# Kernel optimization log

Measured on AMD Instinct MI355X. Metric: run time of the kernel, lower is better.

Reference implementation:

```python
import jax, jax.numpy as jnp
import numpy as np

N = 1_000_000  # total_voxels
V = 128        # volume_size


def setup_inputs() -> dict:
    key = jax.random.key(0)
    ks = jax.random.split(key, 10)
    inds = jax.random.randint(ks[0], (N, 3), 0, V, dtype=jnp.int32)
    reference_values = jax.random.normal(ks[1], (1, N), dtype=jnp.float32)
    # SIREN-ish init scales: ~1/sqrt(fan_in) keeps sin() inputs O(1); tiny final
    # layer scale keeps delta_coords sub-voxel (as training would).
    W0 = jax.random.normal(ks[2], (3 * N, 8), dtype=jnp.float32) / np.float32(np.sqrt(3 * N))
    W1 = jax.random.normal(ks[3], (8, 8), dtype=jnp.float32) / np.float32(np.sqrt(8))
    W2 = jax.random.normal(ks[4], (8, 8), dtype=jnp.float32) / np.float32(np.sqrt(8))
    W3 = jax.random.normal(ks[5], (8, 8), dtype=jnp.float32) / np.float32(np.sqrt(8))
    W4 = jax.random.normal(ks[6], (8, 8), dtype=jnp.float32) / np.float32(np.sqrt(8))
    W5 = jax.random.normal(ks[7], (8, 4 * N), dtype=jnp.float32) * np.float32(0.01 / np.sqrt(8))
    z8 = jnp.zeros((8,), jnp.float32)
    return {
        "inds": inds, "reference_values": reference_values,
        "W0": W0, "b0": z8, "W1": W1, "b1": z8, "W2": W2, "b2": z8,
        "W3": W3, "b3": z8, "W4": W4, "b4": z8,
        "W5": W5, "b5": jnp.zeros((4 * N,), jnp.float32),
        "volume_size": V,
    }


def reference(inds, reference_values, W0, b0, W1, b1, W2, b2, W3, b3, W4, b4,
              W5, b5, volume_size):
    n = inds.shape[0]
    factor = 0.5 * volume_size
    # normalized coords buffer: stack (z,y,x) columns -> (1, N, 3) in [-1, 1)
    coords_n = (jnp.stack([inds[:, 2], inds[:, 1], inds[:, 0]], axis=1)[None]
                .astype(jnp.float32) - factor) / factor
    # tiny SIREN MLP on the flattened coord vector (1, 3N)
    x = jnp.sin(coords_n.reshape(1, -1) @ W0 + b0)
    for W, b in ((W1, b1), (W2, b2), (W3, b3), (W4, b4)):
        x = x + jnp.sin(x @ W + b)
    x = (x @ W5 + b5).reshape(1, n, 4)          # (1, N, 4)
    delta_coords, delta_values = x[..., :3], x[..., 3]
    values = jax.nn.relu(reference_values + delta_values)      # (1, N)
    coords = factor * (coords_n + delta_coords) + factor       # voxel-space, (1, N, 3)
    # trilinear 8-corner splat
    bposf = jnp.floor(coords)
    bposi = bposf.astype(jnp.int32)                             # (1, N, 3)
    f = coords - bposf
    fx, fy, fz = f[..., 0], f[..., 1], f[..., 2]
    gx, gy, gz = 1.0 - fx, 1.0 - fy, 1.0 - fz
    bamp = jnp.concatenate([
        values * gx * gy * gz, values * fx * gy * gz,
        values * gx * fy * gz, values * gx * gy * fz,
        values * gx * fy * fz, values * fx * gy * fz,
        values * fx * fy * gz, values * fx * fy * fz,
    ], axis=1)                                                  # (1, 8N)
    offs = jnp.array([[0, 0, 0], [1, 0, 0], [0, 1, 0], [0, 0, 1],
                      [0, 1, 1], [1, 0, 1], [1, 1, 0], [1, 1, 1]], jnp.int32)
    bpos = jnp.concatenate([bposi + o for o in offs], axis=1)   # (1, 8N, 3)
    vol0 = jnp.zeros((values.shape[0], volume_size, volume_size, volume_size),
                     jnp.float32)

    def scatter(vol, p, a):  # out-of-bounds corners are dropped (jax default)
        return vol.at[p[:, 2], p[:, 1], p[:, 0]].add(a)

    return jax.vmap(scatter, in_axes=(0, 0, 0))(vol0, bpos, bamp)
```

## Files before the change

### kernel.cpp

```cpp
#include <hip/hip_runtime.h>
#include <hip/hip_bf16.h>

constexpr int V = 128;
constexpr int NTILES = 512;
constexpr int TD = 17;
constexpr int TSIZE = TD * TD * TD;
constexpr int NS = 16;
constexpr int CAPS = 256;
constexpr int CNT_INTS = NS * NTILES * 16;

typedef float __attribute__((ext_vector_type(4))) f4_t;
__device__ __forceinline__ f4_t ldnt(const float* p) {
  return __builtin_nontemporal_load((const f4_t*)p);
}

__global__ __launch_bounds__(256) void k_reduce_w0(
    const int* __restrict__ inds, const float* __restrict__ W0,
    float* __restrict__ partials, float4* __restrict__ vol4,
    int4* __restrict__ cnt4, int threeN) {
  int g = blockIdx.x * 256 + threadIdx.x;
  vol4[g] = make_float4(0.f, 0.f, 0.f, 0.f);
  if (cnt4 && g < CNT_INTS / 4) cnt4[g] = make_int4(0, 0, 0, 0);

  float acc[8];
#pragma unroll
  for (int k = 0; k < 8; ++k) acc[k] = 0.f;

  int stride = gridDim.x * blockDim.x;
  for (int j = g; j < threeN; j += stride) {
    int c = j % 3;
    float cval = ((float)inds[j + 2 - 2 * c] - 64.0f) * 0.015625f;
    const float* w = W0 + (size_t)j * 8;
    f4_t a = ldnt(w);
    f4_t b = ldnt(w + 4);
    acc[0] += cval * a.x; acc[1] += cval * a.y;
    acc[2] += cval * a.z; acc[3] += cval * a.w;
    acc[4] += cval * b.x; acc[5] += cval * b.y;
    acc[6] += cval * b.z; acc[7] += cval * b.w;
  }

#pragma unroll
  for (int off = 32; off > 0; off >>= 1) {
#pragma unroll
    for (int k = 0; k < 8; ++k) acc[k] += __shfl_down(acc[k], off);
  }

  __shared__ float red[4][8];
  int wave = threadIdx.x >> 6;
  int lane = threadIdx.x & 63;
  if (lane == 0) {
#pragma unroll
    for (int k = 0; k < 8; ++k) red[wave][k] = acc[k];
  }
  __syncthreads();
  if (threadIdx.x < 8) {
    int k = threadIdx.x;
    partials[(size_t)blockIdx.x * 8 + k] = red[0][k] + red[1][k] + red[2][k] + red[3][k];
  }
}

__global__ __launch_bounds__(256) void k_mlp(
    const float* __restrict__ partials, int nb,
    const float* __restrict__ b0,
    const float* __restrict__ W1, const float* __restrict__ b1,
    const float* __restrict__ W2, const float* __restrict__ b2,
    const float* __restrict__ W3, const float* __restrict__ b3,
    const float* __restrict__ W4, const float* __restrict__ b4,
    float* __restrict__ x8_out) {
  __shared__ float red[256];
  __shared__ float accv[8];
  int tid = threadIdx.x;
  int k = tid & 7;
  float s = 0.f;
  for (int b = tid >> 3; b < nb; b += 32) s += partials[(size_t)b * 8 + k];
  red[tid] = s;
  __syncthreads();
  if (tid < 8) {
    float t = 0.f;
    for (int j = tid; j < 256; j += 8) t += red[j];
    accv[tid] = t;
  }
  __syncthreads();
  if (tid == 0) {
    float x[8];
#pragma unroll
    for (int kk = 0; kk < 8; ++kk) x[kk] = sinf(accv[kk] + b0[kk]);
    const float* Ws[4] = {W1, W2, W3, W4};
    const float* bs[4] = {b1, b2, b3, b4};
    for (int l = 0; l < 4; ++l) {
      float t[8];
#pragma unroll
      for (int kk = 0; kk < 8; ++kk) {
        float ss = bs[l][kk];
#pragma unroll
        for (int j = 0; j < 8; ++j) ss += x[j] * Ws[l][j * 8 + kk];
        t[kk] = ss;
      }
#pragma unroll
      for (int kk = 0; kk < 8; ++kk) x[kk] += sinf(t[kk]);
    }
#pragma unroll
    for (int kk = 0; kk < 8; ++kk) x8_out[kk] = x[kk];
  }
}

__device__ inline int tile_of(float cx, float cy, float cz) {
  int bx = (int)floorf(cx), by = (int)floorf(cy), bz = (int)floorf(cz);
  int tx = min(max(bx, 0), V - 1) >> 4;
  int ty = min(max(by, 0), V - 1) >> 4;
  int tz = min(max(bz, 0), V - 1) >> 4;
  return (tz << 6) | (ty << 3) | tx;
}

__device__ inline void scatter_direct(float* vol, float cx, float cy, float cz,
                                      float value) {
  float bxf = floorf(cx), byf = floorf(cy), bzf = floorf(cz);
  int bx = (int)bxf, by = (int)byf, bz = (int)bzf;
  float fx = cx - bxf, fy = cy - byf, fz = cz - bzf;
  float gx = 1.f - fx, gy = 1.f - fy, gz = 1.f - fz;
#pragma unroll
  for (int dz = 0; dz < 2; ++dz)
#pragma unroll
    for (int dy = 0; dy < 2; ++dy)
#pragma unroll
      for (int dx = 0; dx < 2; ++dx) {
        float w = value * (dx ? fx : gx) * (dy ? fy : gy) * (dz ? fz : gz);
        int px = bx + dx, py = by + dy, pz = bz + dz;
        if (px < 0) px += V;
        if (py < 0) py += V;
        if (pz < 0) pz += V;
        if ((unsigned)px < (unsigned)V && (unsigned)py < (unsigned)V &&
            (unsigned)pz < (unsigned)V)
          atomicAdd(vol + ((size_t)pz * V * V + (size_t)py * V + px), w);
      }
}

__global__ __launch_bounds__(256) void k_decode_scatter(
    const int* __restrict__ inds, const float* __restrict__ refv,
    const float* __restrict__ W5, const float* __restrict__ b5,
    const float* __restrict__ x8_buf, float4* __restrict__ srt,
    int* __restrict__ cnt, float* __restrict__ vol, int N) {
  __shared__ float x8[8];
  if (threadIdx.x < 8) x8[threadIdx.x] = x8_buf[threadIdx.x];
  __syncthreads();

  int i = blockIdx.x * 256 + threadIdx.x;
  if (i >= N) return;

  const size_t fourN = (size_t)4 * N;
  f4_t o = ldnt(b5 + (size_t)4 * i);
  float out0 = o.x, out1 = o.y, out2 = o.z, out3 = o.w;
#pragma unroll
  for (int k = 0; k < 8; ++k) {
    float xv = x8[k];
    f4_t w = ldnt(W5 + (size_t)k * fourN + (size_t)4 * i);
    out0 += xv * w.x; out1 += xv * w.y; out2 += xv * w.z; out3 += xv * w.w;
  }
  float value = refv[i] + out3;
  value = value > 0.f ? value : 0.f;
  if (value <= 0.f) return;

  int i0 = inds[3 * i], i1 = inds[3 * i + 1], i2 = inds[3 * i + 2];
  float cx = (((float)i2 - 64.0f) * 0.015625f + out0) * 64.0f + 64.0f;
  float cy = (((float)i1 - 64.0f) * 0.015625f + out1) * 64.0f + 64.0f;
  float cz = (((float)i0 - 64.0f) * 0.015625f + out2) * 64.0f + 64.0f;

  int t = tile_of(cx, cy, cz);
  int s = blockIdx.x & (NS - 1);
  int slot = s * NTILES + t;
  int pos = atomicAdd(&cnt[slot * 16], 1);
  if (pos < CAPS) {
    srt[(size_t)slot * CAPS + pos] = make_float4(cx, cy, cz, value);
  } else {
    scatter_direct(vol, cx, cy, cz, value);
  }
}

__global__ __launch_bounds__(256) void k_tile_fused(
    const float4* __restrict__ srt, const int* __restrict__ cnt,
    float* __restrict__ vol) {
  __shared__ float tl[TSIZE];
  __shared__ int scnt_sh[NS];
  int t = blockIdx.x;
  int ox = (t & 7) << 4, oy = ((t >> 3) & 7) << 4, oz = (t >> 6) << 4;
  for (int j = threadIdx.x; j < TSIZE; j += 256) tl[j] = 0.f;
  if (threadIdx.x < NS) {
    int slot = threadIdx.x * NTILES + t;
    scnt_sh[threadIdx.x] = min(cnt[slot * 16], CAPS);
  }
  __syncthreads();

  int cb[NS];
  int total = 0;
#pragma unroll
  for (int k = 0; k < NS; ++k) { cb[k] = total; total += scnt_sh[k]; }

  for (int i = threadIdx.x; i < total; i += 256) {
    int s = 0, base = 0;
#pragma unroll
    for (int k = 1; k < NS; ++k) {
      bool ge = (i >= cb[k]);
      s = ge ? k : s;
      base = ge ? cb[k] : base;
    }
    float4 r = srt[((size_t)(s * NTILES + t)) * CAPS + (i - base)];

    float bxf = floorf(r.x), byf = floorf(r.y), bzf = floorf(r.z);
    int bx = (int)bxf, by = (int)byf, bz = (int)bzf;
    float fx = r.x - bxf, fy = r.y - byf, fz = r.z - bzf;
    float gx = 1.f - fx, gy = 1.f - fy, gz = 1.f - fz;
    float value = r.w;

#pragma unroll
    for (int dz = 0; dz < 2; ++dz) {
#pragma unroll
      for (int dy = 0; dy < 2; ++dy) {
#pragma unroll
        for (int dx = 0; dx < 2; ++dx) {
          float w = value * (dx ? fx : gx) * (dy ? fy : gy) * (dz ? fz : gz);
          int px = bx + dx, py = by + dy, pz = bz + dz;
          if (px < 0) px += V;
          if (py < 0) py += V;
          if (pz < 0) pz += V;
          if (px >= V || py >= V || pz >= V) continue;
          int lx = px - ox, ly = py - oy, lz = pz - oz;
          if ((unsigned)lx < (unsigned)TD && (unsigned)ly < (unsigned)TD &&
              (unsigned)lz < (unsigned)TD) {
            atomicAdd(&tl[lz * (TD * TD) + ly * TD + lx], w);
          } else {
            atomicAdd(vol + ((size_t)pz * V * V + (size_t)py * V + px), w);
          }
        }
      }
    }
  }
  __syncthreads();

  for (int j = threadIdx.x; j < TSIZE; j += 256) {
    float v = tl[j];
    if (v != 0.f) {
      int lz = j / (TD * TD);
      int rem = j - lz * (TD * TD);
      int ly = rem / TD;
      int lx = rem - ly * TD;
      int px = ox + lx, py = oy + ly, pz = oz + lz;
      if (px < V && py < V && pz < V)
        atomicAdd(vol + ((size_t)pz * V * V + (size_t)py * V + px), v);
    }
  }
}

__global__ __launch_bounds__(256) void k_scatter(
    const int* __restrict__ inds, const float* __restrict__ refv,
    const float* __restrict__ W5, const float* __restrict__ b5,
    const float* __restrict__ x8_buf, float* __restrict__ vol, int N) {
  __shared__ float x8[8];
  if (threadIdx.x < 8) x8[threadIdx.x] = x8_buf[threadIdx.x];
  __syncthreads();
  int i = blockIdx.x * blockDim.x + threadIdx.x;
  if (i >= N) return;
  const size_t fourN = (size_t)4 * N;
  float4 o = *(const float4*)(b5 + (size_t)4 * i);
  float out0 = o.x, out1 = o.y, out2 = o.z, out3 = o.w;
#pragma unroll
  for (int k = 0; k < 8; ++k) {
    float xv = x8[k];
    float4 w = *(const float4*)(W5 + (size_t)k * fourN + (size_t)4 * i);
    out0 += xv * w.x; out1 += xv * w.y; out2 += xv * w.z; out3 += xv * w.w;
  }
  float value = refv[i] + out3;
  value = value > 0.f ? value : 0.f;
  int i0 = inds[3 * i], i1 = inds[3 * i + 1], i2 = inds[3 * i + 2];
  float cx = (((float)i2 - 64.0f) * 0.015625f + out0) * 64.0f + 64.0f;
  float cy = (((float)i1 - 64.0f) * 0.015625f + out1) * 64.0f + 64.0f;
  float cz = (((float)i0 - 64.0f) * 0.015625f + out2) * 64.0f + 64.0f;
  scatter_direct(vol, cx, cy, cz, value);
}

extern "C" void kernel_launch(void* const* d_in, const int* in_sizes, int n_in,
                              void* d_out, int out_size, void* d_ws, size_t ws_size,
                              hipStream_t stream) {
  const int*   inds = (const int*)d_in[0];
  const float* refv = (const float*)d_in[1];
  const float* W0   = (const float*)d_in[2];
  const float* b0   = (const float*)d_in[3];
  const float* W1   = (const float*)d_in[4];
  const float* b1   = (const float*)d_in[5];
  const float* W2   = (const float*)d_in[6];
  const float* b2   = (const float*)d_in[7];
  const float* W3   = (const float*)d_in[8];
  const float* b3   = (const float*)d_in[9];
  const float* W4   = (const float*)d_in[10];
  const float* b4   = (const float*)d_in[11];
  const float* W5   = (const float*)d_in[12];
  const float* b5   = (const float*)d_in[13];

  int N = in_sizes[0] / 3;
  float* vol = (float*)d_out;
  char* w = (char*)d_ws;

  const int NB_R = 2048;
  float*  x8       = (float*)(w + 0);
  float*  partials = (float*)(w + 256);
  int*    cnt      = (int*)(w + 131072);
  float4* srt      = (float4*)(w + 1048576);

  size_t needed = (size_t)1048576 + (size_t)NS * NTILES * CAPS * 16;

  if (ws_size >= needed) {
    k_reduce_w0<<<NB_R, 256, 0, stream>>>(inds, W0, partials, (float4*)vol,
                                          (int4*)cnt, 3 * N);
    k_mlp<<<1, 256, 0, stream>>>(partials, NB_R, b0, W1, b1, W2, b2, W3, b3, W4, b4, x8);
    k_decode_scatter<<<(N + 255) / 256, 256, 0, stream>>>(inds, refv, W5, b5, x8,
                                                          srt, cnt, vol, N);
    k_tile_fused<<<NTILES, 256, 0, stream>>>(srt, cnt, vol);
  } else {
    hipMemsetAsync(d_out, 0, (size_t)out_size * sizeof(float), stream);
    k_reduce_w0<<<NB_R, 256, 0, stream>>>(inds, W0, partials, (float4*)vol,
                                          (int4*)nullptr, 3 * N);
    k_mlp<<<1, 256, 0, stream>>>(partials, NB_R, b0, W1, b1, W2, b2, W3, b3, W4, b4, x8);
    k_scatter<<<(N + 255) / 256, 256, 0, stream>>>(inds, refv, W5, b5, x8, vol, N);
  }
}
```

Measured before the change: 341.4 us.

## Move negative-wrap corners to decode, use plain stores for tile interiors, widen tile blocks

Corners that wrap from negative coordinates are now splatted with global atomics in the decode kernel, so the tile kernel only handles non-negative corners inside its 17^3 halo tile and never issues global atomics in its inner loop. Interior cells of each tile, which no other tile touches, are written back with a plain read-modify-write instead of an atomic. Halo cells still use atomics. The tile kernel also moves from 256 to 512 threads per block. The plain write relies on every contribution to an interior cell coming from that tile, including decode-time fallback atomics, which finish before the tile kernel runs.

Result: slower. 369.6 us (+8.3%).

```diff
diff --git a/kernel.cpp b/kernel.cpp
--- a/kernel.cpp
+++ b/kernel.cpp
@@ -171,19 +171,41 @@
   int pos = atomicAdd(&cnt[slot * 16], 1);
   if (pos < CAPS) {
     srt[(size_t)slot * CAPS + pos] = make_float4(cx, cy, cz, value);
+    if (cx < 0.f || cy < 0.f || cz < 0.f) {
+      float bxf = floorf(cx), byf = floorf(cy), bzf = floorf(cz);
+      int bx = (int)bxf, by = (int)byf, bz = (int)bzf;
+      float fx = cx - bxf, fy = cy - byf, fz = cz - bzf;
+      float gx = 1.f - fx, gy = 1.f - fy, gz = 1.f - fz;
+#pragma unroll
+      for (int dz = 0; dz < 2; ++dz)
+#pragma unroll
+        for (int dy = 0; dy < 2; ++dy)
+#pragma unroll
+          for (int dx = 0; dx < 2; ++dx) {
+            int px = bx + dx, py = by + dy, pz = bz + dz;
+            if (px >= 0 && py >= 0 && pz >= 0) continue;
+            float w = value * (dx ? fx : gx) * (dy ? fy : gy) * (dz ? fz : gz);
+            if (px < 0) px += V;
+            if (py < 0) py += V;
+            if (pz < 0) pz += V;
+            if ((unsigned)px < (unsigned)V && (unsigned)py < (unsigned)V &&
+                (unsigned)pz < (unsigned)V)
+              atomicAdd(vol + ((size_t)pz * V * V + (size_t)py * V + px), w);
+          }
+    }
   } else {
     scatter_direct(vol, cx, cy, cz, value);
   }
 }
 
-__global__ __launch_bounds__(256) void k_tile_fused(
+__global__ __launch_bounds__(512) void k_tile_fused(
     const float4* __restrict__ srt, const int* __restrict__ cnt,
     float* __restrict__ vol) {
   __shared__ float tl[TSIZE];
   __shared__ int scnt_sh[NS];
   int t = blockIdx.x;
   int ox = (t & 7) << 4, oy = ((t >> 3) & 7) << 4, oz = (t >> 6) << 4;
-  for (int j = threadIdx.x; j < TSIZE; j += 256) tl[j] = 0.f;
+  for (int j = threadIdx.x; j < TSIZE; j += 512) tl[j] = 0.f;
   if (threadIdx.x < NS) {
     int slot = threadIdx.x * NTILES + t;
     scnt_sh[threadIdx.x] = min(cnt[slot * 16], CAPS);
@@ -195,7 +217,7 @@
 #pragma unroll
   for (int k = 0; k < NS; ++k) { cb[k] = total; total += scnt_sh[k]; }
 
-  for (int i = threadIdx.x; i < total; i += 256) {
+  for (int i = threadIdx.x; i < total; i += 512) {
     int s = 0, base = 0;
 #pragma unroll
     for (int k = 1; k < NS; ++k) {
@@ -219,33 +241,30 @@
         for (int dx = 0; dx < 2; ++dx) {
           float w = value * (dx ? fx : gx) * (dy ? fy : gy) * (dz ? fz : gz);
           int px = bx + dx, py = by + dy, pz = bz + dz;
-          if (px < 0) px += V;
-          if (py < 0) py += V;
-          if (pz < 0) pz += V;
-          if (px >= V || py >= V || pz >= V) continue;
+          if (px < 0 || py < 0 || pz < 0) continue;
           int lx = px - ox, ly = py - oy, lz = pz - oz;
-          if ((unsigned)lx < (unsigned)TD && (unsigned)ly < (unsigned)TD &&
-              (unsigned)lz < (unsigned)TD) {
-            atomicAdd(&tl[lz * (TD * TD) + ly * TD + lx], w);
-          } else {
-            atomicAdd(vol + ((size_t)pz * V * V + (size_t)py * V + px), w);
-          }
+          if (lx > 16 || ly > 16 || lz > 16) continue;
+          atomicAdd(&tl[lz * (TD * TD) + ly * TD + lx], w);
         }
       }
     }
   }
   __syncthreads();
 
-  for (int j = threadIdx.x; j < TSIZE; j += 256) {
+  for (int j = threadIdx.x; j < TSIZE; j += 512) {
     float v = tl[j];
-    if (v != 0.f) {
-      int lz = j / (TD * TD);
-      int rem = j - lz * (TD * TD);
-      int ly = rem / TD;
-      int lx = rem - ly * TD;
-      int px = ox + lx, py = oy + ly, pz = oz + lz;
-      if (px < V && py < V && pz < V)
-        atomicAdd(vol + ((size_t)pz * V * V + (size_t)py * V + px), v);
+    int lz = j / (TD * TD);
+    int rem = j - lz * (TD * TD);
+    int ly = rem / TD;
+    int lx = rem - ly * TD;
+    int px = ox + lx, py = oy + ly, pz = oz + lz;
+    size_t idx = (size_t)pz * V * V + (size_t)py * V + px;
+    bool interior = ((unsigned)(lx - 1) < 15u) && ((unsigned)(ly - 1) < 15u) &&
+                    ((unsigned)(lz - 1) < 15u);
+    if (interior) {
+      vol[idx] += v;
+    } else if (v != 0.f && px < V && py < V && pz < V) {
+      atomicAdd(vol + idx, v);
     }
   }
 }
@@ -313,7 +332,7 @@
     k_mlp<<<1, 256, 0, stream>>>(partials, NB_R, b0, W1, b1, W2, b2, W3, b3, W4, b4, x8);
     k_decode_scatter<<<(N + 255) / 256, 256, 0, stream>>>(inds, refv, W5, b5, x8,
                                                           srt, cnt, vol, N);
-    k_tile_fused<<<NTILES, 256, 0, stream>>>(srt, cnt, vol);
+    k_tile_fused<<<NTILES, 512, 0, stream>>>(srt, cnt, vol);
   } else {
     hipMemsetAsync(d_out, 0, (size_t)out_size * sizeof(float), stream);
     k_reduce_w0<<<NB_R, 256, 0, stream>>>(inds, W0, partials, (float4*)vol,
```
